# Kernel optimization log

Measured on AMD Instinct MI355X. Metric: run time of the kernel, lower is better.

The kernel has to match this reference:

```python
import jax, jax.numpy as jnp
import numpy as np
from jax import lax

SEQ, BATCH, IN, HID = 4096, 8, 1024, 1024


def setup_inputs() -> dict:
    key = jax.random.key(0)
    k1, k2 = jax.random.split(key)
    X = jax.random.normal(k1, (SEQ, BATCH, IN), dtype=jnp.float32)
    hidden = jnp.zeros((BATCH, HID), dtype=jnp.float32)  # None init == zeros
    W = jax.random.normal(k2, (3 * HID, IN), dtype=jnp.float32) * 0.02
    b = jnp.zeros((3 * HID,), dtype=jnp.float32)
    return {"X": X, "hidden": hidden, "W": W, "b": b}


def reference(X, hidden, W, b):
    # window=1: source = X; Y = Linear(X) -> [S, B, 3H]
    Y = jnp.einsum('sbi,hi->sbh', X, W) + b
    Z, F, O = jnp.split(Y, 3, axis=2)
    Z = jnp.tanh(Z)
    F = jax.nn.sigmoid(F)

    # ForgetMult: c_t = f_t * z_t + (1 - f_t) * c_{t-1}
    def step(c, fz):
        f, z = fz
        c = f * z + (1.0 - f) * c
        return c, c

    _, C = lax.scan(step, hidden, (F, Z))  # C: [S, B, H]
    H = jax.nn.sigmoid(O) * C
    return (H, C[-1:, :, :], C)
```

## Files before the change

### kernel.cpp

```cpp
#include <hip/hip_runtime.h>
#include <hip/hip_bf16.h>
#include <stdint.h>

#define S_   4096
#define B_   8
#define IN_  1024
#define H_   1024
#define M_   (S_ * B_)
#define N_   (3 * H_)
#define K_   IN_
#define CH_  (B_ * H_)
#define NC_  64
#define T_   (S_ / NC_)

typedef unsigned short u16;
typedef __bf16 bf16x8 __attribute__((ext_vector_type(8)));
typedef float  f32x4  __attribute__((ext_vector_type(4)));

__device__ __forceinline__ u16 f2bf(float f) {
  unsigned u = __float_as_uint(f);
  u += 0x7fffu + ((u >> 16) & 1u);
  return (u16)(u >> 16);
}

__device__ __forceinline__ float sigmoid_(float x) { return 1.0f / (1.0f + __expf(-x)); }
__device__ __forceinline__ float tanh_(float x)    { return 2.0f / (1.0f + __expf(-2.0f * x)) - 1.0f; }

__global__ void cvt_bf16_kernel(const float* __restrict__ in, u16* __restrict__ out, int n8) {
  int i = blockIdx.x * blockDim.x + threadIdx.x;
  if (i >= n8) return;
  const float4* p = (const float4*)in;
  float4 a = p[2 * i], b = p[2 * i + 1];
  alignas(16) u16 us[8] = {f2bf(a.x), f2bf(a.y), f2bf(a.z), f2bf(a.w),
                           f2bf(b.x), f2bf(b.y), f2bf(b.z), f2bf(b.w)};
  ((uint4*)out)[i] = *(const uint4*)us;
}

__global__ void gemm_act(const u16* __restrict__ Ab, const u16* __restrict__ Bb,
                         const float* __restrict__ bias,
                         float* __restrict__ zt,
                         float* __restrict__ Cf,
                         float* __restrict__ Ho) {
  __shared__ alignas(16) u16 As[128 * 64];
  __shared__ alignas(16) u16 Bs[128 * 64];
  const int t = threadIdx.x;
  const int w = t >> 6, l = t & 63;
  const int d  = blockIdx.y * gridDim.x + blockIdx.x;
  const int wk = (d & 7) * ((N_ / 128) * (M_ / 128) / 8) + (d >> 3);
  const int m0 = (wk / (N_ / 128)) * 128;
  const int n0 = (wk % (N_ / 128)) * 128;
  const int wm = (w & 1) * 64, wn = (w >> 1) * 64;
  const int r  = l & 15;
  const int ko = (l >> 4) * 8;
  const int lrow = l >> 3;
  const int lcol = (l & 7) * 8;

  f32x4 acc[4][4];
#pragma unroll
  for (int i = 0; i < 4; ++i)
#pragma unroll
    for (int j = 0; j < 4; ++j) acc[i][j] = (f32x4){0.f, 0.f, 0.f, 0.f};

  for (int k0 = 0; k0 < K_; k0 += 64) {
    __syncthreads();
#pragma unroll
    for (int s = 0; s < 4; ++s) {
      const int q = w * 4 + s;
      const u16* ga = Ab + (size_t)(m0 + q * 8 + lrow) * K_ + k0 + lcol;
      const u16* gb = Bb + (size_t)(n0 + q * 8 + lrow) * K_ + k0 + lcol;
      __builtin_amdgcn_global_load_lds((const __attribute__((address_space(1))) void*)ga,
                                       (__attribute__((address_space(3))) void*)(As + q * 512),
                                       16, 0, 0);
      __builtin_amdgcn_global_load_lds((const __attribute__((address_space(1))) void*)gb,
                                       (__attribute__((address_space(3))) void*)(Bs + q * 512),
                                       16, 0, 0);
    }
    __syncthreads();
#pragma unroll
    for (int kk = 0; kk < 64; kk += 32) {
      bf16x8 af[4], bfr[4];
#pragma unroll
      for (int i = 0; i < 4; ++i) af[i]  = *(const bf16x8*)(As + (wm + i * 16 + r) * 64 + kk + ko);
#pragma unroll
      for (int j = 0; j < 4; ++j) bfr[j] = *(const bf16x8*)(Bs + (wn + j * 16 + r) * 64 + kk + ko);
#pragma unroll
      for (int i = 0; i < 4; ++i)
#pragma unroll
        for (int j = 0; j < 4; ++j)
          acc[i][j] = __builtin_amdgcn_mfma_f32_16x16x32_bf16(af[i], bfr[j], acc[i][j], 0, 0, 0);
    }
  }

  const int seg = n0 >> 10;
  const int nh0 = (n0 & 1023) + wn;
  float* dst = (seg == 0) ? zt : (seg == 1 ? Cf : Ho);
#pragma unroll
  for (int i = 0; i < 4; ++i) {
#pragma unroll
    for (int j = 0; j < 4; ++j) {
      const int nn = nh0 + j * 16 + (l & 15);
      const float bv = bias[seg * 1024 + nn];
#pragma unroll
      for (int rr = 0; rr < 4; ++rr) {
        const int mm = m0 + wm + i * 16 + (l >> 4) * 4 + rr;
        const float v = acc[i][j][rr] + bv;
        const float av = (seg == 0) ? tanh_(v) : sigmoid_(v);
        dst[(size_t)mm * H_ + nn] = av;
      }
    }
  }
}

__global__ void scanA(const float* __restrict__ Cf, const float* __restrict__ zt,
                      float* __restrict__ ckA, float* __restrict__ ckC) {
  const int ch2 = blockIdx.x * 256 + threadIdx.x;
  const int j   = blockIdx.y;
  size_t base2 = (size_t)j * T_ * (CH_ / 2) + ch2;
  const float2* Cf2 = (const float2*)Cf;
  const float2* zt2 = (const float2*)zt;
  float2 A = {1.f, 1.f}, c = {0.f, 0.f};
  for (int tt = 0; tt < T_; ++tt) {
    const float2 f = Cf2[base2];
    const float2 z = zt2[base2];
    const float omx = 1.f - f.x, omy = 1.f - f.y;
    c.x = f.x * z.x + omx * c.x;
    c.y = f.y * z.y + omy * c.y;
    A.x *= omx;
    A.y *= omy;
    base2 += CH_ / 2;
  }
  ((float2*)ckA)[(size_t)j * (CH_ / 2) + ch2] = A;
  ((float2*)ckC)[(size_t)j * (CH_ / 2) + ch2] = c;
}

__global__ void scanComb(const float* __restrict__ ckA, const float* __restrict__ ckC,
                         const float* __restrict__ hidden, float* __restrict__ carry) {
  const int ch = blockIdx.x * 64 + threadIdx.x;
  float c = hidden[ch];
  for (int j = 0; j < NC_; ++j) {
    carry[j * CH_ + ch] = c;
    c = ckC[j * CH_ + ch] + ckA[j * CH_ + ch] * c;
  }
}

__global__ void scanB(float* __restrict__ Cf,
                      const float* __restrict__ zt,
                      float* __restrict__ Ho,
                      float* __restrict__ Clast,
                      const float* __restrict__ carry) {
  const int ch2 = blockIdx.x * 256 + threadIdx.x;
  const int j   = blockIdx.y;
  size_t base2 = (size_t)j * T_ * (CH_ / 2) + ch2;
  float2* Cf2 = (float2*)Cf;
  const float2* zt2 = (const float2*)zt;
  float2* Ho2 = (float2*)Ho;
  float2 c = ((const float2*)carry)[(size_t)j * (CH_ / 2) + ch2];
  for (int tt = 0; tt < T_; ++tt) {
    const float2 f  = Cf2[base2];
    const float2 z  = zt2[base2];
    const float2 so = Ho2[base2];
    c.x = f.x * z.x + (1.f - f.x) * c.x;
    c.y = f.y * z.y + (1.f - f.y) * c.y;
    Cf2[base2] = c;
    Ho2[base2] = float2{so.x * c.x, so.y * c.y};
    base2 += CH_ / 2;
  }
  if (j == NC_ - 1) ((float2*)Clast)[ch2] = c;
}

extern "C" void kernel_launch(void* const* d_in, const int* in_sizes, int n_in,
                              void* d_out, int out_size, void* d_ws, size_t ws_size,
                              hipStream_t stream) {
  const float* X    = (const float*)d_in[0];
  const float* hid  = (const float*)d_in[1];
  const float* W    = (const float*)d_in[2];
  const float* bias = (const float*)d_in[3];

  float* out   = (float*)d_out;
  float* Ho    = out;
  float* Clast = out + (size_t)M_ * H_;
  float* Cf    = Clast + CH_;

  char* ws = (char*)d_ws;
  u16*  Xb    = (u16*)ws;
  u16*  Wb    = (u16*)(ws + 67108864);
  float* zt   = (float*)(ws + 73400320);
  float* ckA  = (float*)(ws + 207618048);
  float* ckC  = (float*)(ws + 209715200);
  float* carry= (float*)(ws + 211812352);

  cvt_bf16_kernel<<<(M_ * K_ / 8 + 255) / 256, 256, 0, stream>>>(X, Xb, M_ * K_ / 8);
  cvt_bf16_kernel<<<(N_ * K_ / 8 + 255) / 256, 256, 0, stream>>>(W, Wb, N_ * K_ / 8);
  gemm_act<<<dim3(N_ / 128, M_ / 128), 256, 0, stream>>>(Xb, Wb, bias, zt, Cf, Ho);
  scanA<<<dim3(CH_ / 512, NC_), 256, 0, stream>>>(Cf, zt, ckA, ckC);
  scanComb<<<CH_ / 64, 64, 0, stream>>>(ckA, ckC, hid, carry);
  scanB<<<dim3(CH_ / 512, NC_), 256, 0, stream>>>(Cf, zt, Ho, Clast, carry);
}
```

Measured before the change: 779.1 us.

## Rewrite GEMM as 256x256 tile, 8-wave, multi-buffered LDS pipeline with swizzle

```diff
diff --git a/kernel.cpp b/kernel.cpp
--- a/kernel.cpp
+++ b/kernel.cpp
@@ -36,76 +36,148 @@
   ((uint4*)out)[i] = *(const uint4*)us;
 }
 
-__global__ void gemm_act(const u16* __restrict__ Ab, const u16* __restrict__ Bb,
-                         const float* __restrict__ bias,
-                         float* __restrict__ zt,
-                         float* __restrict__ Cf,
-                         float* __restrict__ Ho) {
-  __shared__ alignas(16) u16 As[128 * 64];
-  __shared__ alignas(16) u16 Bs[128 * 64];
-  const int t = threadIdx.x;
-  const int w = t >> 6, l = t & 63;
-  const int d  = blockIdx.y * gridDim.x + blockIdx.x;
-  const int wk = (d & 7) * ((N_ / 128) * (M_ / 128) / 8) + (d >> 3);
-  const int m0 = (wk / (N_ / 128)) * 128;
-  const int n0 = (wk % (N_ / 128)) * 128;
-  const int wm = (w & 1) * 64, wn = (w >> 1) * 64;
-  const int r  = l & 15;
-  const int ko = (l >> 4) * 8;
-  const int lrow = l >> 3;
-  const int lcol = (l & 7) * 8;
-
-  f32x4 acc[4][4];
-#pragma unroll
-  for (int i = 0; i < 4; ++i)
-#pragma unroll
-    for (int j = 0; j < 4; ++j) acc[i][j] = (f32x4){0.f, 0.f, 0.f, 0.f};
-
-  for (int k0 = 0; k0 < K_; k0 += 64) {
-    __syncthreads();
-#pragma unroll
-    for (int s = 0; s < 4; ++s) {
-      const int q = w * 4 + s;
-      const u16* ga = Ab + (size_t)(m0 + q * 8 + lrow) * K_ + k0 + lcol;
-      const u16* gb = Bb + (size_t)(n0 + q * 8 + lrow) * K_ + k0 + lcol;
-      __builtin_amdgcn_global_load_lds((const __attribute__((address_space(1))) void*)ga,
-                                       (__attribute__((address_space(3))) void*)(As + q * 512),
-                                       16, 0, 0);
-      __builtin_amdgcn_global_load_lds((const __attribute__((address_space(1))) void*)gb,
-                                       (__attribute__((address_space(3))) void*)(Bs + q * 512),
-                                       16, 0, 0);
-    }
-    __syncthreads();
-#pragma unroll
-    for (int kk = 0; kk < 64; kk += 32) {
-      bf16x8 af[4], bfr[4];
-#pragma unroll
-      for (int i = 0; i < 4; ++i) af[i]  = *(const bf16x8*)(As + (wm + i * 16 + r) * 64 + kk + ko);
-#pragma unroll
-      for (int j = 0; j < 4; ++j) bfr[j] = *(const bf16x8*)(Bs + (wn + j * 16 + r) * 64 + kk + ko);
-#pragma unroll
-      for (int i = 0; i < 4; ++i)
-#pragma unroll
-        for (int j = 0; j < 4; ++j)
-          acc[i][j] = __builtin_amdgcn_mfma_f32_16x16x32_bf16(af[i], bfr[j], acc[i][j], 0, 0, 0);
-    }
-  }
+#define SWZ(x) ((x) ^ (((x) >> 3) & 0x30))
+
+#define DS_A(s, h, mh) do {                                                    \
+  const char* base_ = (const char*)As_[(s)*2+(h)];                             \
+  af[0] = *(const bf16x8*)(base_ + aoff[mh][0]);                               \
+  af[1] = *(const bf16x8*)(base_ + aoff[mh][1]);                               \
+  af[2] = *(const bf16x8*)(base_ + aoff[mh][2]);                               \
+  af[3] = *(const bf16x8*)(base_ + aoff[mh][3]);                               \
+} while (0)
+
+#define DS_B(s, h) do {                                                        \
+  const char* base_ = (const char*)Bs_[(s)*2+(h)];                             \
+  bfr[0] = *(const bf16x8*)(base_ + boff[0]);                                  \
+  bfr[1] = *(const bf16x8*)(base_ + boff[1]);                                  \
+  bfr[2] = *(const bf16x8*)(base_ + boff[2]);                                  \
+  bfr[3] = *(const bf16x8*)(base_ + boff[3]);                                  \
+} while (0)
+
+#define MMA(mh) do {                                                           \
+  __builtin_amdgcn_s_setprio(1);                                              \
+  _Pragma("unroll")                                                            \
+  for (int fi_ = 0; fi_ < 4; ++fi_)                                            \
+    _Pragma("unroll")                                                          \
+    for (int fj_ = 0; fj_ < 4; ++fj_)                                          \
+      acc[(mh)*4+fi_][fj_] = __builtin_amdgcn_mfma_f32_16x16x32_bf16(          \
+          af[fi_], bfr[fj_], acc[(mh)*4+fi_][fj_], 0, 0, 0);                   \
+  __builtin_amdgcn_s_setprio(0);                                              \
+} while (0)
+
+#define PH_SYNC() do {                                                         \
+  asm volatile("" ::: "memory");                                               \
+  __builtin_amdgcn_s_barrier();                                                \
+  asm volatile("s_waitcnt lgkmcnt(0)" ::: "memory");                           \
+} while (0)
+
+#define PH_END() do {                                                          \
+  asm volatile("" ::: "memory");                                               \
+  __builtin_amdgcn_s_barrier();                                                \
+} while (0)
+
+#define VW(n) asm volatile("s_waitcnt vmcnt(" #n ")" ::: "memory")
+
+__global__ __launch_bounds__(512, 2) void gemm_act(
+    const u16* __restrict__ Ab, const u16* __restrict__ Bb,
+    const float* __restrict__ bias,
+    float* __restrict__ zt,
+    float* __restrict__ Cf,
+    float* __restrict__ Ho) {
+  __shared__ alignas(16) u16 As_[4][8192];
+  __shared__ alignas(16) u16 Bs_[4][8192];
+
+  const int tid = threadIdx.x;
+  const int w = tid >> 6, l = tid & 63;
+  const int m0 = blockIdx.y * 256, n0 = blockIdx.x * 256;
+  const int wmo = (w >> 2) * 128, wno = (w & 3) * 64;
+  const int lr = l & 15, lq = l >> 4;
+
+  const int D0b  = w * 1024 + l * 16;
+  const int row0 = D0b >> 6;
+  const int c0   = (SWZ(D0b) & 63) >> 1;
+
+  int aoff[2][4], boff[4];
+#pragma unroll
+  for (int mh = 0; mh < 2; ++mh)
+#pragma unroll
+    for (int fi = 0; fi < 4; ++fi)
+      aoff[mh][fi] = SWZ((wmo + (mh * 4 + fi) * 16 + lr) * 64 + lq * 16);
+#pragma unroll
+  for (int fj = 0; fj < 4; ++fj)
+    boff[fj] = SWZ((wno + fj * 16 + lr) * 64 + lq * 16);
+
+  auto stage = [&](const u16* __restrict__ G, int rb, int tt, int hh, u16* dstp) {
+    const u16* s0 = G + (size_t)(rb + row0) * K_ + (tt * 64 + hh * 32 + c0);
+    __builtin_amdgcn_global_load_lds(
+        (const __attribute__((address_space(1))) void*)s0,
+        (__attribute__((address_space(3))) void*)(dstp + (D0b >> 1)), 16, 0, 0);
+    const u16* s1 = s0 + (size_t)128 * K_;
+    __builtin_amdgcn_global_load_lds(
+        (const __attribute__((address_space(1))) void*)s1,
+        (__attribute__((address_space(3))) void*)(dstp + (D0b >> 1) + 4096), 16, 0, 0);
+  };
+
+  f32x4 acc[8][4] = {};
+  bf16x8 af[4], bfr[4];
+
+  stage(Ab, m0, 0, 0, As_[0]); stage(Bb, n0, 0, 0, Bs_[0]);
+  stage(Ab, m0, 0, 1, As_[1]); stage(Bb, n0, 0, 1, Bs_[1]);
+  stage(Ab, m0, 1, 0, As_[2]); stage(Bb, n0, 1, 0, Bs_[2]);
+  VW(4);
+  PH_END();
+
+  for (int i = 0; i < 7; ++i) {
+    const int t1 = 2 * i + 1, t2 = 2 * i + 2, t3 = 2 * i + 3;
+    DS_A(0, 0, 0); DS_B(0, 0); stage(Ab, m0, t1, 1, As_[3]);
+    PH_SYNC(); MMA(0); PH_END();
+    DS_A(0, 0, 1);             stage(Bb, n0, t1, 1, Bs_[3]);
+    PH_SYNC(); MMA(1); PH_END();
+    DS_A(0, 1, 0); DS_B(0, 1); stage(Ab, m0, t2, 0, As_[0]);
+    PH_SYNC(); MMA(0); PH_END();
+    DS_A(0, 1, 1);             stage(Bb, n0, t2, 0, Bs_[0]); VW(4);
+    PH_SYNC(); MMA(1); PH_END();
+    DS_A(1, 0, 0); DS_B(1, 0); stage(Ab, m0, t2, 1, As_[1]);
+    PH_SYNC(); MMA(0); PH_END();
+    DS_A(1, 0, 1);             stage(Bb, n0, t2, 1, Bs_[1]);
+    PH_SYNC(); MMA(1); PH_END();
+    DS_A(1, 1, 0); DS_B(1, 1); stage(Ab, m0, t3, 0, As_[2]);
+    PH_SYNC(); MMA(0); PH_END();
+    DS_A(1, 1, 1);             stage(Bb, n0, t3, 0, Bs_[2]); VW(4);
+    PH_SYNC(); MMA(1); PH_END();
+  }
+
+  DS_A(0, 0, 0); DS_B(0, 0); stage(Ab, m0, 15, 1, As_[3]);
+  PH_SYNC(); MMA(0); PH_END();
+  DS_A(0, 0, 1);             stage(Bb, n0, 15, 1, Bs_[3]);
+  PH_SYNC(); MMA(1); PH_END();
+  DS_A(0, 1, 0); DS_B(0, 1);
+  PH_SYNC(); MMA(0); PH_END();
+  DS_A(0, 1, 1); VW(0);
+  PH_SYNC(); MMA(1); PH_END();
+  DS_A(1, 0, 0); DS_B(1, 0);
+  PH_SYNC(); MMA(0); PH_END();
+  DS_A(1, 0, 1);
+  PH_SYNC(); MMA(1); PH_END();
+  DS_A(1, 1, 0); DS_B(1, 1);
+  PH_SYNC(); MMA(0); PH_END();
+  DS_A(1, 1, 1);
+  PH_SYNC(); MMA(1); PH_END();
 
   const int seg = n0 >> 10;
-  const int nh0 = (n0 & 1023) + wn;
+  const int nh0 = (n0 & 1023) + wno;
   float* dst = (seg == 0) ? zt : (seg == 1 ? Cf : Ho);
 #pragma unroll
-  for (int i = 0; i < 4; ++i) {
-#pragma unroll
-    for (int j = 0; j < 4; ++j) {
-      const int nn = nh0 + j * 16 + (l & 15);
-      const float bv = bias[seg * 1024 + nn];
+  for (int fj = 0; fj < 4; ++fj) {
+    const int nn = nh0 + fj * 16 + lr;
+    const float bv = bias[seg * 1024 + nn];
+#pragma unroll
+    for (int fi = 0; fi < 8; ++fi) {
 #pragma unroll
       for (int rr = 0; rr < 4; ++rr) {
-        const int mm = m0 + wm + i * 16 + (l >> 4) * 4 + rr;
-        const float v = acc[i][j][rr] + bv;
-        const float av = (seg == 0) ? tanh_(v) : sigmoid_(v);
-        dst[(size_t)mm * H_ + nn] = av;
+        const int mm = m0 + wmo + fi * 16 + lq * 4 + rr;
+        const float v = acc[fi][fj][rr] + bv;
+        dst[(size_t)mm * H_ + nn] = (seg == 0) ? tanh_(v) : sigmoid_(v);
       }
     }
   }
@@ -191,7 +263,7 @@
 
   cvt_bf16_kernel<<<(M_ * K_ / 8 + 255) / 256, 256, 0, stream>>>(X, Xb, M_ * K_ / 8);
   cvt_bf16_kernel<<<(N_ * K_ / 8 + 255) / 256, 256, 0, stream>>>(W, Wb, N_ * K_ / 8);
-  gemm_act<<<dim3(N_ / 128, M_ / 128), 256, 0, stream>>>(Xb, Wb, bias, zt, Cf, Ho);
+  gemm_act<<<dim3(N_ / 256, M_ / 256), 512, 0, stream>>>(Xb, Wb, bias, zt, Cf, Ho);
   scanA<<<dim3(CH_ / 512, NC_), 256, 0, stream>>>(Cf, zt, ckA, ckC);
   scanComb<<<CH_ / 64, 64, 0, stream>>>(ckA, ckC, hid, carry);
   scanB<<<dim3(CH_ / 512, NC_), 256, 0, stream>>>(Cf, zt, Ho, Clast, carry);
```

New measurement: 797.6 us. +2.4%, slower.
